# Performance work log

Hardware: AMD Instinct MI355X
Metric: run time of the kernel (lower is better)

The kernel has to match this reference:

```python
import jax, jax.numpy as jnp
import numpy as np

LN_EPS = 1e-3  # keras LayerNormalization default epsilon


def _layernorm(x, gamma, beta):
    mu = jnp.mean(x, axis=-1, keepdims=True)
    var = jnp.mean(jnp.square(x - mu), axis=-1, keepdims=True)
    return (x - mu) * jax.lax.rsqrt(var + LN_EPS) * gamma + beta


def setup_inputs() -> dict:
    key = jax.random.key(0)
    ks = jax.random.split(key, 8)
    B, H, W, C = 4, 64, 64, 256
    units = 256
    s = 1.0 / np.sqrt(C)  # he-normal-ish scale for 1x1 convs
    return {
        "inputs": jax.random.normal(ks[0], (B, H, W, C), jnp.float32),
        "context": jax.random.normal(ks[1], (B, H, W, C), jnp.float32),
        "Wq": jax.random.normal(ks[2], (C, units), jnp.float32) * s,
        "bq": jnp.zeros((units,), jnp.float32),
        "Wk": jax.random.normal(ks[3], (C, units), jnp.float32) * s,
        "bk": jnp.zeros((units,), jnp.float32),
        "Wv": jax.random.normal(ks[4], (C, units), jnp.float32) * s,
        "bv": jnp.zeros((units,), jnp.float32),
        "Wp": jax.random.normal(ks[5], (units, units), jnp.float32) * s,
        "bp": jnp.zeros((units,), jnp.float32),
        "gamma": jnp.ones((C,), jnp.float32),
        "beta": jnp.zeros((C,), jnp.float32),
    }


def reference(inputs, context, Wq, bq, Wk, bk, Wv, bv, Wp, bp, gamma, beta):
    B, H, W, C = inputs.shape
    units = Wq.shape[1]
    scale = jnp.float32(units) ** -0.5

    x_n = _layernorm(inputs, gamma, beta)          # normalized inputs (also residual base)
    q = jnp.einsum('bhwc,cu->bhwu', x_n, Wq) + bq   # [B,H,W,U]
    k = jnp.einsum('bhwc,cu->bhwu', context, Wk) + bk
    v = jnp.einsum('bhwc,cu->bhwu', context, Wv) + bv

    # full (h*w) x (H*W) score tensor, as in the original
    scores = jnp.einsum('bhwc,bHWc->bhwHW', q, k) * scale
    scores = scores.reshape(B, H, W, H * W)
    attn = jax.nn.softmax(scores, axis=-1).reshape(B, H, W, H, W)

    out = jnp.einsum('bhwHW,bHWc->bhwc', attn, v)
    proj = jnp.einsum('bhwc,cu->bhwu', out, Wp) + bp
    return x_n + proj
```

## Files before the change

### kernel.cpp

```cpp
#include <hip/hip_runtime.h>

typedef short v8s __attribute__((ext_vector_type(8)));
typedef float v4f __attribute__((ext_vector_type(4)));
using u16 = unsigned short;

#define QSCALE 0.09016844f

__device__ __forceinline__ u16 f2b(float f) {
  union { float f; unsigned u; } v; v.f = f;
  unsigned r = v.u + 0x7FFFu + ((v.u >> 16) & 1u);
  return (u16)(r >> 16);
}

__global__ void ln_prep(const float* __restrict__ x, const float* __restrict__ ctx,
                        const float* __restrict__ gamma, const float* __restrict__ beta,
                        float* __restrict__ xn_f, u16* __restrict__ xn_b,
                        u16* __restrict__ ctx_b)
{
  const int tid = threadIdx.x;
  const int wid = tid >> 6, lane = tid & 63;
  const int row = blockIdx.x * 4 + wid;
  const size_t tidx = ((size_t)(row >> 4) * 8 + (lane >> 3)) * 512 +
                      (((lane >> 1) & 3) * 16 + (row & 15)) * 8 + (lane & 1) * 4;
  if (blockIdx.y == 0) {
    const float4 xv = *(const float4*)(x + (size_t)row * 256 + lane * 4);
    float s1 = xv.x + xv.y + xv.z + xv.w;
    float s2 = xv.x*xv.x + xv.y*xv.y + xv.z*xv.z + xv.w*xv.w;
#pragma unroll
    for (int m = 32; m >= 1; m >>= 1) {
      s1 += __shfl_xor(s1, m);
      s2 += __shfl_xor(s2, m);
    }
    const float mu  = s1 * (1.0f/256.0f);
    const float var = s2 * (1.0f/256.0f) - mu*mu;
    const float rs  = rsqrtf(var + 1e-3f);
    const float4 g = *(const float4*)(gamma + lane*4);
    const float4 b = *(const float4*)(beta  + lane*4);
    float4 y;
    y.x = (xv.x-mu)*rs*g.x + b.x;
    y.y = (xv.y-mu)*rs*g.y + b.y;
    y.z = (xv.z-mu)*rs*g.z + b.z;
    y.w = (xv.w-mu)*rs*g.w + b.w;
    *(float4*)(xn_f + (size_t)row*256 + lane*4) = y;
    ushort4 yb; yb.x=f2b(y.x); yb.y=f2b(y.y); yb.z=f2b(y.z); yb.w=f2b(y.w);
    *(ushort4*)(xn_b + tidx) = yb;
  } else {
    const float4 cv = *(const float4*)(ctx + (size_t)row * 256 + lane * 4);
    ushort4 cb; cb.x=f2b(cv.x); cb.y=f2b(cv.y); cb.z=f2b(cv.z); cb.w=f2b(cv.w);
    *(ushort4*)(ctx_b + tidx) = cb;
  }
}

__global__ void wtrans(const float* __restrict__ wq, const float* __restrict__ wk,
                       const float* __restrict__ wv, const float* __restrict__ wp,
                       u16* __restrict__ tq, u16* __restrict__ tk,
                       u16* __restrict__ tv, u16* __restrict__ tp)
{
  const float* src; u16* dst; float scl = 1.0f;
  switch (blockIdx.y) {
    case 0:  src = wq; dst = tq; scl = QSCALE; break;
    case 1:  src = wk; dst = tk; break;
    case 2:  src = wv; dst = tv; break;
    default: src = wp; dst = tp; break;
  }
  const int t  = threadIdx.x;
  const int kk = blockIdx.x * 16 + (t >> 4);
  const int n0 = (t & 15) * 16;
  const size_t base = (size_t)((t & 15) * 8 + (kk >> 5)) * 512 +
                      ((kk >> 3) & 3) * 16 * 8 + (kk & 7);
#pragma unroll
  for (int j = 0; j < 16; j++)
    dst[base + (size_t)j * 8] = f2b(src[(size_t)kk * 256 + n0 + j] * scl);
}

__global__ __launch_bounds__(256) void gemm_qkv(
    const u16* __restrict__ xn_b, const u16* __restrict__ ctx_b,
    const u16* __restrict__ wqt, const u16* __restrict__ wkt, const u16* __restrict__ wvt,
    const float* __restrict__ bq, const float* __restrict__ bk, const float* __restrict__ bv,
    u16* __restrict__ qo, u16* __restrict__ ko, u16* __restrict__ vto)
{
  const int mode = blockIdx.y;
  const u16* A; const u16* Wt; const float* bias;
  if (mode == 0)      { A = xn_b;  Wt = wqt; bias = bq; }
  else if (mode == 1) { A = ctx_b; Wt = wkt; bias = bk; }
  else                { A = ctx_b; Wt = wvt; bias = bv; }
  const float bscale = (mode == 0) ? QSCALE : 1.0f;
  const int wid = threadIdx.x >> 6, lane = threadIdx.x & 63;
  const int lm = lane & 15, q4 = lane >> 4;
  const int m0 = blockIdx.x * 64 + wid * 16;
  const u16* abase = A + (size_t)(m0 >> 4) * 4096 + lane * 8;
  v8s af[8];
#pragma unroll
  for (int kf = 0; kf < 8; kf++) af[kf] = *(const v8s*)(abase + kf * 512);
#pragma unroll
  for (int ct = 0; ct < 16; ct++) {
    const int c = ct * 16 + lm;
    const u16* wbase = Wt + (size_t)ct * 4096 + lane * 8;
    v8s wf[8];
#pragma unroll
    for (int kf = 0; kf < 8; kf++) wf[kf] = *(const v8s*)(wbase + kf * 512);
    v4f a0 = {0.f,0.f,0.f,0.f}, a1 = a0, a2 = a0, a3 = a0;
    a0 = __builtin_amdgcn_mfma_f32_16x16x32_bf16(af[0], wf[0], a0, 0, 0, 0);
    a1 = __builtin_amdgcn_mfma_f32_16x16x32_bf16(af[2], wf[2], a1, 0, 0, 0);
    a2 = __builtin_amdgcn_mfma_f32_16x16x32_bf16(af[4], wf[4], a2, 0, 0, 0);
    a3 = __builtin_amdgcn_mfma_f32_16x16x32_bf16(af[6], wf[6], a3, 0, 0, 0);
    a0 = __builtin_amdgcn_mfma_f32_16x16x32_bf16(af[1], wf[1], a0, 0, 0, 0);
    a1 = __builtin_amdgcn_mfma_f32_16x16x32_bf16(af[3], wf[3], a1, 0, 0, 0);
    a2 = __builtin_amdgcn_mfma_f32_16x16x32_bf16(af[5], wf[5], a2, 0, 0, 0);
    a3 = __builtin_amdgcn_mfma_f32_16x16x32_bf16(af[7], wf[7], a3, 0, 0, 0);
    const v4f acc = (a0 + a1) + (a2 + a3);
    const float bb = bias[c] * bscale;
    if (mode == 2) {
      const int b = m0 >> 12;
      const int chunk = (m0 & 4095) >> 6;
      const int kic = (m0 & 63) + q4 * 4;
      const int ks = kic >> 5;
      const int q4p = (kic >> 3) & 3;
      const size_t idx = ((size_t)(b * 64 + chunk) * 32 + (c >> 4) * 2 + ks) * 512 +
                         (q4p * 16 + (c & 15)) * 8 + (q4 & 1) * 4;
      ushort4 pk;
      pk.x = f2b(acc[0] + bb); pk.y = f2b(acc[1] + bb);
      pk.z = f2b(acc[2] + bb); pk.w = f2b(acc[3] + bb);
      *(ushort4*)(vto + idx) = pk;
    } else {
      u16* out = (mode == 0) ? qo : ko;
      const size_t base = ((size_t)(m0 >> 4) * 8 + (c >> 5)) * 512 +
                          (((c >> 3) & 3) * 16 + q4 * 4) * 8 + (c & 7);
#pragma unroll
      for (int r = 0; r < 4; r++)
        out[base + (size_t)r * 8] = f2b(acc[r] + bb);
    }
  }
}

__global__ __launch_bounds__(256, 2) void attn_kernel(
    const u16* __restrict__ q, const u16* __restrict__ k,
    const u16* __restrict__ vt, u16* __restrict__ ao)
{
  __shared__ u16 P[2][32][72];
  __shared__ float Lp[4][32];
  __shared__ float Lt[32];
  const int bid  = blockIdx.x;
  const int b    = (bid & 7) >> 1;
  const int qblk = ((bid >> 3) << 1) | (bid & 1);
  const int tid = threadIdx.x;
  const int w   = tid >> 6, lane = tid & 63;
  const int lm  = lane & 15, q4 = lane >> 4;
  const int m0  = qblk * 32;
  const u16* qb = q  + (size_t)b * 1048576;
  const u16* kb = k  + (size_t)b * 1048576;
  const u16* vb = vt + (size_t)b * 1048576;

  v8s qf[2][8];
#pragma unroll
  for (int qt = 0; qt < 2; qt++) {
    const u16* qbase = qb + (size_t)((m0 >> 4) + qt) * 4096 + lane * 8;
#pragma unroll
    for (int kf = 0; kf < 8; kf++) qf[qt][kf] = *(const v8s*)(qbase + kf * 512);
  }

  v4f o[2][4];
#pragma unroll
  for (int qt = 0; qt < 2; qt++)
#pragma unroll
    for (int ct = 0; ct < 4; ct++) o[qt][ct] = (v4f){0.f, 0.f, 0.f, 0.f};
  float lsum[2] = {0.f, 0.f};

  v8s kfr[8];
  {
    const u16* kbase = kb + (size_t)w * 4096 + lane * 8;
#pragma unroll
    for (int kf = 0; kf < 8; kf++) kfr[kf] = *(const v8s*)(kbase + kf * 512);
  }

  for (int s0 = 0; s0 < 4096; s0 += 64) {
    const int pb = (s0 >> 6) & 1;
    const int chunk = s0 >> 6;
    v8s vfr[4][2];
#pragma unroll
    for (int ct = 0; ct < 4; ct++) {
      const u16* vbase = vb + ((size_t)chunk * 32 + (w * 4 + ct) * 2) * 512 + lane * 8;
      vfr[ct][0] = *(const v8s*)(vbase);
      vfr[ct][1] = *(const v8s*)(vbase + 512);
    }
    v4f sc[2];
#pragma unroll
    for (int qt = 0; qt < 2; qt++) sc[qt] = (v4f){0.f, 0.f, 0.f, 0.f};
#pragma unroll
    for (int kf = 0; kf < 8; kf++)
#pragma unroll
      for (int qt = 0; qt < 2; qt++)
        sc[qt] = __builtin_amdgcn_mfma_f32_16x16x32_bf16(kfr[kf], qf[qt][kf], sc[qt], 0, 0, 0);
    {
      const int sn = (s0 + 64) & 4095;
      const u16* kbase = kb + (size_t)((sn >> 4) + w) * 4096 + lane * 8;
#pragma unroll
      for (int kf = 0; kf < 8; kf++) kfr[kf] = *(const v8s*)(kbase + kf * 512);
    }
#pragma unroll
    for (int qt = 0; qt < 2; qt++) {
      const float e0 = exp2f(sc[qt][0]);
      const float e1 = exp2f(sc[qt][1]);
      const float e2 = exp2f(sc[qt][2]);
      const float e3 = exp2f(sc[qt][3]);
      lsum[qt] += (e0 + e1) + (e2 + e3);
      unsigned d0, d1;
      asm("v_cvt_pk_bf16_f32 %0, %1, %2" : "=v"(d0) : "v"(e0), "v"(e1));
      asm("v_cvt_pk_bf16_f32 %0, %1, %2" : "=v"(d1) : "v"(e2), "v"(e3));
      uint2 pk; pk.x = d0; pk.y = d1;
      *(uint2*)(&P[pb][qt * 16 + lm][w * 16 + q4 * 4]) = pk;
    }
    __syncthreads();
#pragma unroll
    for (int qt = 0; qt < 2; qt++) {
      const v8s pf0 = *(const v8s*)(&P[pb][qt * 16 + lm][q4 * 8]);
      const v8s pf1 = *(const v8s*)(&P[pb][qt * 16 + lm][32 + q4 * 8]);
#pragma unroll
      for (int ct = 0; ct < 4; ct++) {
        o[qt][ct] = __builtin_amdgcn_mfma_f32_16x16x32_bf16(pf0, vfr[ct][0], o[qt][ct], 0, 0, 0);
        o[qt][ct] = __builtin_amdgcn_mfma_f32_16x16x32_bf16(pf1, vfr[ct][1], o[qt][ct], 0, 0, 0);
      }
    }
  }

#pragma unroll
  for (int qt = 0; qt < 2; qt++) {
    float t = lsum[qt];
    t += __shfl_xor(t, 16);
    t += __shfl_xor(t, 32);
    lsum[qt] = t;
  }
  if (q4 == 0) {
#pragma unroll
    for (int qt = 0; qt < 2; qt++) Lp[w][qt * 16 + lm] = lsum[qt];
  }
  __syncthreads();
  if (tid < 32) Lt[tid] = Lp[0][tid] + Lp[1][tid] + Lp[2][tid] + Lp[3][tid];
  __syncthreads();

  const int rstrip0 = (b * 4096 + m0) >> 4;
#pragma unroll
  for (int qt = 0; qt < 2; qt++)
#pragma unroll
    for (int r = 0; r < 4; r++) {
      const float linv = 1.0f / Lt[qt * 16 + q4 * 4 + r];
#pragma unroll
      for (int ct = 0; ct < 4; ct++) {
        const int ch = w * 64 + ct * 16 + lm;
        const size_t idx = ((size_t)(rstrip0 + qt) * 8 + (ch >> 5)) * 512 +
                           (((ch >> 3) & 3) * 16 + q4 * 4 + r) * 8 + (ch & 7);
        ao[idx] = f2b(o[qt][ct][r] * linv);
      }
    }
}

__global__ __launch_bounds__(256) void gemm_proj(
    const u16* __restrict__ A, const u16* __restrict__ Wt, const float* __restrict__ bias,
    const float* __restrict__ xn_f, float* __restrict__ out)
{
  const int wid = threadIdx.x >> 6, lane = threadIdx.x & 63;
  const int lm = lane & 15, q4 = lane >> 4;
  const int m0 = blockIdx.x * 64 + wid * 16;
  const u16* abase = A + (size_t)(m0 >> 4) * 4096 + lane * 8;
  v8s af[8];
#pragma unroll
  for (int kf = 0; kf < 8; kf++) af[kf] = *(const v8s*)(abase + kf * 512);
#pragma unroll
  for (int ct = 0; ct < 16; ct++) {
    const int c = ct * 16 + lm;
    const u16* wbase = Wt + (size_t)ct * 4096 + lane * 8;
    v8s wf[8];
#pragma unroll
    for (int kf = 0; kf < 8; kf++) wf[kf] = *(const v8s*)(wbase + kf * 512);
    v4f a0 = {0.f,0.f,0.f,0.f}, a1 = a0, a2 = a0, a3 = a0;
    a0 = __builtin_amdgcn_mfma_f32_16x16x32_bf16(af[0], wf[0], a0, 0, 0, 0);
    a1 = __builtin_amdgcn_mfma_f32_16x16x32_bf16(af[2], wf[2], a1, 0, 0, 0);
    a2 = __builtin_amdgcn_mfma_f32_16x16x32_bf16(af[4], wf[4], a2, 0, 0, 0);
    a3 = __builtin_amdgcn_mfma_f32_16x16x32_bf16(af[6], wf[6], a3, 0, 0, 0);
    a0 = __builtin_amdgcn_mfma_f32_16x16x32_bf16(af[1], wf[1], a0, 0, 0, 0);
    a1 = __builtin_amdgcn_mfma_f32_16x16x32_bf16(af[3], wf[3], a1, 0, 0, 0);
    a2 = __builtin_amdgcn_mfma_f32_16x16x32_bf16(af[5], wf[5], a2, 0, 0, 0);
    a3 = __builtin_amdgcn_mfma_f32_16x16x32_bf16(af[7], wf[7], a3, 0, 0, 0);
    const v4f acc = (a0 + a1) + (a2 + a3);
    const float bb = bias[c];
#pragma unroll
    for (int r = 0; r < 4; r++) {
      const size_t idx = (size_t)(m0 + q4 * 4 + r) * 256 + c;
      out[idx] = xn_f[idx] + acc[r] + bb;
    }
  }
}

extern "C" void kernel_launch(void* const* d_in, const int* in_sizes, int n_in,
                              void* d_out, int out_size, void* d_ws, size_t ws_size,
                              hipStream_t stream)
{
  (void)in_sizes; (void)n_in; (void)out_size; (void)ws_size;
  const float* inputs  = (const float*)d_in[0];
  const float* context = (const float*)d_in[1];
  const float* Wq = (const float*)d_in[2];
  const float* bq = (const float*)d_in[3];
  const float* Wk = (const float*)d_in[4];
  const float* bk = (const float*)d_in[5];
  const float* Wv = (const float*)d_in[6];
  const float* bv = (const float*)d_in[7];
  const float* Wp = (const float*)d_in[8];
  const float* bp = (const float*)d_in[9];
  const float* gamma = (const float*)d_in[10];
  const float* beta  = (const float*)d_in[11];
  float* out = (float*)d_out;

  char* p = (char*)d_ws;
  float* xn_f = (float*)p; p += (size_t)16384 * 256 * 4;
  u16* xn_b   = (u16*)p;   p += (size_t)16384 * 256 * 2;
  u16* ctx_b  = (u16*)p;   p += (size_t)16384 * 256 * 2;
  u16* qbuf   = (u16*)p;   p += (size_t)16384 * 256 * 2;
  u16* kbuf   = (u16*)p;   p += (size_t)16384 * 256 * 2;
  u16* vtbuf  = (u16*)p;   p += (size_t)16384 * 256 * 2;
  u16* wqt = (u16*)p; p += (size_t)256 * 256 * 2;
  u16* wkt = (u16*)p; p += (size_t)256 * 256 * 2;
  u16* wvt = (u16*)p; p += (size_t)256 * 256 * 2;
  u16* wpt = (u16*)p; p += (size_t)256 * 256 * 2;
  u16* aobuf = xn_b;

  ln_prep<<<dim3(4096, 2), 256, 0, stream>>>(inputs, context, gamma, beta, xn_f, xn_b, ctx_b);
  wtrans<<<dim3(16, 4), 256, 0, stream>>>(Wq, Wk, Wv, Wp, wqt, wkt, wvt, wpt);
  gemm_qkv<<<dim3(256, 3), 256, 0, stream>>>(xn_b, ctx_b, wqt, wkt, wvt, bq, bk, bv, qbuf, kbuf, vtbuf);
  attn_kernel<<<dim3(512), 256, 0, stream>>>(qbuf, kbuf, vtbuf, aobuf);
  gemm_proj<<<dim3(256), 256, 0, stream>>>(aobuf, wpt, bp, xn_f, out);
}
```

Measured before the change: 224.7 us.

## Enlarge attention tile to 64 queries by 128 keys with 8 waves

```diff
diff --git a/kernel.cpp b/kernel.cpp
--- a/kernel.cpp
+++ b/kernel.cpp
@@ -133,38 +133,38 @@
   }
 }
 
-__global__ __launch_bounds__(256, 2) void attn_kernel(
+__global__ __launch_bounds__(512, 2) void attn_kernel(
     const u16* __restrict__ q, const u16* __restrict__ k,
     const u16* __restrict__ vt, u16* __restrict__ ao)
 {
-  __shared__ u16 P[2][32][72];
-  __shared__ float Lp[4][32];
-  __shared__ float Lt[32];
+  __shared__ u16 P[2][64][136];
+  __shared__ float Lp[8][64];
+  __shared__ float Lt[64];
   const int bid  = blockIdx.x;
   const int b    = (bid & 7) >> 1;
   const int qblk = ((bid >> 3) << 1) | (bid & 1);
-  const int tid = threadIdx.x;
-  const int w   = tid >> 6, lane = tid & 63;
-  const int lm  = lane & 15, q4 = lane >> 4;
-  const int m0  = qblk * 32;
+  const int tid  = threadIdx.x;
+  const int w    = tid >> 6, lane = tid & 63;
+  const int lm   = lane & 15, q4 = lane >> 4;
+  const int m0   = qblk * 64;
   const u16* qb = q  + (size_t)b * 1048576;
   const u16* kb = k  + (size_t)b * 1048576;
   const u16* vb = vt + (size_t)b * 1048576;
 
-  v8s qf[2][8];
-#pragma unroll
-  for (int qt = 0; qt < 2; qt++) {
+  v8s qf[4][8];
+#pragma unroll
+  for (int qt = 0; qt < 4; qt++) {
     const u16* qbase = qb + (size_t)((m0 >> 4) + qt) * 4096 + lane * 8;
 #pragma unroll
     for (int kf = 0; kf < 8; kf++) qf[qt][kf] = *(const v8s*)(qbase + kf * 512);
   }
 
-  v4f o[2][4];
-#pragma unroll
-  for (int qt = 0; qt < 2; qt++)
-#pragma unroll
-    for (int ct = 0; ct < 4; ct++) o[qt][ct] = (v4f){0.f, 0.f, 0.f, 0.f};
-  float lsum[2] = {0.f, 0.f};
+  v4f o[4][2];
+#pragma unroll
+  for (int qt = 0; qt < 4; qt++)
+#pragma unroll
+    for (int ct = 0; ct < 2; ct++) o[qt][ct] = (v4f){0.f, 0.f, 0.f, 0.f};
+  float lsum[4] = {0.f, 0.f, 0.f, 0.f};
 
   v8s kfr[8];
   {
@@ -173,32 +173,33 @@
     for (int kf = 0; kf < 8; kf++) kfr[kf] = *(const v8s*)(kbase + kf * 512);
   }
 
-  for (int s0 = 0; s0 < 4096; s0 += 64) {
-    const int pb = (s0 >> 6) & 1;
-    const int chunk = s0 >> 6;
-    v8s vfr[4][2];
-#pragma unroll
-    for (int ct = 0; ct < 4; ct++) {
-      const u16* vbase = vb + ((size_t)chunk * 32 + (w * 4 + ct) * 2) * 512 + lane * 8;
-      vfr[ct][0] = *(const v8s*)(vbase);
-      vfr[ct][1] = *(const v8s*)(vbase + 512);
-    }
-    v4f sc[2];
-#pragma unroll
-    for (int qt = 0; qt < 2; qt++) sc[qt] = (v4f){0.f, 0.f, 0.f, 0.f};
+  for (int c128 = 0; c128 < 32; c128++) {
+    const int pb = c128 & 1;
+    v8s vfr[2][4];
+#pragma unroll
+    for (int ct = 0; ct < 2; ct++)
+#pragma unroll
+      for (int j = 0; j < 4; j++) {
+        const size_t tile = (size_t)(c128 * 2 + (j >> 1)) * 32 +
+                            (w * 2 + ct) * 2 + (j & 1);
+        vfr[ct][j] = *(const v8s*)(vb + tile * 512 + lane * 8);
+      }
+    v4f sc[4];
+#pragma unroll
+    for (int qt = 0; qt < 4; qt++) sc[qt] = (v4f){0.f, 0.f, 0.f, 0.f};
 #pragma unroll
     for (int kf = 0; kf < 8; kf++)
 #pragma unroll
-      for (int qt = 0; qt < 2; qt++)
+      for (int qt = 0; qt < 4; qt++)
         sc[qt] = __builtin_amdgcn_mfma_f32_16x16x32_bf16(kfr[kf], qf[qt][kf], sc[qt], 0, 0, 0);
     {
-      const int sn = (s0 + 64) & 4095;
-      const u16* kbase = kb + (size_t)((sn >> 4) + w) * 4096 + lane * 8;
+      const int nc = (c128 + 1) & 31;
+      const u16* kbase = kb + (size_t)(nc * 8 + w) * 4096 + lane * 8;
 #pragma unroll
       for (int kf = 0; kf < 8; kf++) kfr[kf] = *(const v8s*)(kbase + kf * 512);
     }
 #pragma unroll
-    for (int qt = 0; qt < 2; qt++) {
+    for (int qt = 0; qt < 4; qt++) {
       const float e0 = exp2f(sc[qt][0]);
       const float e1 = exp2f(sc[qt][1]);
       const float e2 = exp2f(sc[qt][2]);
@@ -212,19 +213,21 @@
     }
     __syncthreads();
 #pragma unroll
-    for (int qt = 0; qt < 2; qt++) {
-      const v8s pf0 = *(const v8s*)(&P[pb][qt * 16 + lm][q4 * 8]);
-      const v8s pf1 = *(const v8s*)(&P[pb][qt * 16 + lm][32 + q4 * 8]);
-#pragma unroll
-      for (int ct = 0; ct < 4; ct++) {
-        o[qt][ct] = __builtin_amdgcn_mfma_f32_16x16x32_bf16(pf0, vfr[ct][0], o[qt][ct], 0, 0, 0);
-        o[qt][ct] = __builtin_amdgcn_mfma_f32_16x16x32_bf16(pf1, vfr[ct][1], o[qt][ct], 0, 0, 0);
-      }
-    }
-  }
-
-#pragma unroll
-  for (int qt = 0; qt < 2; qt++) {
+    for (int qt = 0; qt < 4; qt++) {
+      v8s pf[4];
+#pragma unroll
+      for (int j = 0; j < 4; j++)
+        pf[j] = *(const v8s*)(&P[pb][qt * 16 + lm][j * 32 + q4 * 8]);
+#pragma unroll
+      for (int ct = 0; ct < 2; ct++)
+#pragma unroll
+        for (int j = 0; j < 4; j++)
+          o[qt][ct] = __builtin_amdgcn_mfma_f32_16x16x32_bf16(pf[j], vfr[ct][j], o[qt][ct], 0, 0, 0);
+    }
+  }
+
+#pragma unroll
+  for (int qt = 0; qt < 4; qt++) {
     float t = lsum[qt];
     t += __shfl_xor(t, 16);
     t += __shfl_xor(t, 32);
@@ -232,21 +235,26 @@
   }
   if (q4 == 0) {
 #pragma unroll
-    for (int qt = 0; qt < 2; qt++) Lp[w][qt * 16 + lm] = lsum[qt];
+    for (int qt = 0; qt < 4; qt++) Lp[w][qt * 16 + lm] = lsum[qt];
   }
   __syncthreads();
-  if (tid < 32) Lt[tid] = Lp[0][tid] + Lp[1][tid] + Lp[2][tid] + Lp[3][tid];
+  if (tid < 64) {
+    float t = 0.f;
+#pragma unroll
+    for (int ww = 0; ww < 8; ww++) t += Lp[ww][tid];
+    Lt[tid] = t;
+  }
   __syncthreads();
 
   const int rstrip0 = (b * 4096 + m0) >> 4;
 #pragma unroll
-  for (int qt = 0; qt < 2; qt++)
+  for (int qt = 0; qt < 4; qt++)
 #pragma unroll
     for (int r = 0; r < 4; r++) {
       const float linv = 1.0f / Lt[qt * 16 + q4 * 4 + r];
 #pragma unroll
-      for (int ct = 0; ct < 4; ct++) {
-        const int ch = w * 64 + ct * 16 + lm;
+      for (int ct = 0; ct < 2; ct++) {
+        const int ch = w * 32 + ct * 16 + lm;
         const size_t idx = ((size_t)(rstrip0 + qt) * 8 + (ch >> 5)) * 512 +
                            (((ch >> 3) & 3) * 16 + q4 * 4 + r) * 8 + (ch & 7);
         ao[idx] = f2b(o[qt][ct][r] * linv);
@@ -326,6 +334,6 @@
   ln_prep<<<dim3(4096, 2), 256, 0, stream>>>(inputs, context, gamma, beta, xn_f, xn_b, ctx_b);
   wtrans<<<dim3(16, 4), 256, 0, stream>>>(Wq, Wk, Wv, Wp, wqt, wkt, wvt, wpt);
   gemm_qkv<<<dim3(256, 3), 256, 0, stream>>>(xn_b, ctx_b, wqt, wkt, wvt, bq, bk, bv, qbuf, kbuf, vtbuf);
-  attn_kernel<<<dim3(512), 256, 0, stream>>>(qbuf, kbuf, vtbuf, aobuf);
+  attn_kernel<<<dim3(256), 512, 0, stream>>>(qbuf, kbuf, vtbuf, aobuf);
   gemm_proj<<<dim3(256), 256, 0, stream>>>(aobuf, wpt, bp, xn_f, out);
 }
```

Measured after the change: 216.7 us. 1.04x faster.
